# Kernel tuning notes

Hardware: AMD Instinct MI355X
Metric: run time of the kernel (lower is better)

The kernel has to match this reference:

```python
import jax, jax.numpy as jnp
import numpy as np

B, N_ROIS, C, H, W = 4, 180, 512, 48, 48
STRIDE = 4
EPS = 1e-5


def _pool_one(feat, roi):
    # feat: [C,H,W], roi: [4] float (y1,x1,y2,x2) in image coords
    r = roi / STRIDE
    r0 = jnp.trunc(r[0]).astype(jnp.int32)
    r1 = jnp.trunc(r[1]).astype(jnp.int32)
    r2 = jnp.ceil(r[2]).astype(jnp.int32)
    r3 = jnp.ceil(r[3]).astype(jnp.int32)
    h_size = r2 - r0 + 1
    w_size = r3 - r1 + 1
    idx2 = jnp.arange(2)
    # AdaptiveMaxPool2d region boundaries: [floor(i*s/2), ceil((i+1)*s/2))
    sh = (idx2 * h_size) // 2
    eh = ((idx2 + 1) * h_size + 1) // 2
    sw = (idx2 * w_size) // 2
    ew = ((idx2 + 1) * w_size + 1) // 2
    hh = jnp.arange(H)[None, :]
    ww = jnp.arange(W)[None, :]
    mask_h = (hh >= (r0 + sh)[:, None]) & (hh < (r0 + eh)[:, None])  # [2,H]
    mask_w = (ww >= (r1 + sw)[:, None]) & (ww < (r1 + ew)[:, None])  # [2,W]
    neg = jnp.finfo(feat.dtype).min
    # max over W within each col region -> [2(oj), C, H]
    mw = jnp.where(mask_w[:, None, None, :], feat[None], neg).max(axis=-1)
    # max over H within each row region -> [2(oi), 2(oj), C]
    p = jnp.where(mask_h[:, None, None, :], mw[None], neg).max(axis=-1)
    # torch layout: [C, oi, oj] then flatten row-major
    return jnp.transpose(p, (2, 0, 1)).reshape(-1)  # [C*4]


def _roi_pool(features, rois):
    # features: [B,C,H,W], rois: [B,N,4] -> [B,N,C*4]
    def per_roi(roi_b):  # roi_b: [B,4]
        return jax.vmap(_pool_one)(features, roi_b)  # [B, C*4]
    out = jax.lax.map(per_roi, jnp.swapaxes(rois, 0, 1))  # [N,B,C*4]
    return jnp.swapaxes(out, 0, 1)


def _bn(x, gamma, beta):
    # training-mode BatchNorm1d over [B, N_ROIS(channels), F]: stats over (B,F)
    mean = x.mean(axis=(0, 2), keepdims=True)
    var = ((x - mean) ** 2).mean(axis=(0, 2), keepdims=True)
    return (x - mean) * jax.lax.rsqrt(var + EPS) * gamma[None, :, None] + beta[None, :, None]


def setup_inputs() -> dict:
    key = jax.random.key(0)
    k1, k2, k3, k4, k5 = jax.random.split(key, 5)
    features = jax.random.normal(k1, (B, C, H, W), dtype=jnp.float32)
    max_coord = (H - 1) * STRIDE
    y = jnp.sort(jax.random.uniform(k2, (B, N_ROIS, 2), minval=0.0, maxval=max_coord), axis=-1)
    x = jnp.sort(jax.random.uniform(k3, (B, N_ROIS, 2), minval=0.0, maxval=max_coord), axis=-1)
    rois = jnp.stack([y[..., 0], x[..., 0], y[..., 1], x[..., 1]], axis=-1)  # [B,N,4]
    F_in = C * 4
    W1 = jax.random.normal(k4, (64, F_in), dtype=jnp.float32) * 0.02
    bl1 = jnp.zeros((64,), dtype=jnp.float32)
    gamma1 = jnp.ones((N_ROIS,), dtype=jnp.float32)
    beta1 = jnp.zeros((N_ROIS,), dtype=jnp.float32)
    gamma2 = jnp.ones((N_ROIS,), dtype=jnp.float32)
    beta2 = jnp.zeros((N_ROIS,), dtype=jnp.float32)
    return {"features": features, "rois": rois, "gamma1": gamma1, "beta1": beta1,
            "W1": W1, "bl1": bl1, "gamma2": gamma2, "beta2": beta2}


def reference(features, rois, gamma1, beta1, W1, bl1, gamma2, beta2):
    pooled = _roi_pool(features, rois)            # [B, 180, 2048]
    x = jax.nn.relu(pooled)
    x = _bn(x, gamma1, beta1)
    y = jnp.einsum('bnf,of->bno', x, W1) + bl1    # [B, 180, 64]
    y = _bn(y, gamma2, beta2)
    return y
```

## Files before the change

### kernel.cpp

```cpp
#include <hip/hip_runtime.h>
#include <hip/hip_bf16.h>
#include <cfloat>
#include <math.h>

#define BB 4
#define NR 180
#define CC 512
#define HH 48
#define WW 48
#define FF (CC*4)
#define OO 64
#define EPSV 1e-5f


typedef unsigned short us2 __attribute__((ext_vector_type(2)));

__device__ __forceinline__ unsigned pmax(unsigned a, unsigned b) {
    return __builtin_bit_cast(unsigned, __builtin_elementwise_max(
        __builtin_bit_cast(us2, a), __builtin_bit_cast(us2, b)));
}
__device__ __forceinline__ uint4 pmax4(uint4 a, uint4 b) {
    return make_uint4(pmax(a.x,b.x), pmax(a.y,b.y), pmax(a.z,b.z), pmax(a.w,b.w));
}
__device__ __forceinline__ unsigned mapb(float f) {
    unsigned fu = __float_as_uint(f);
    unsigned u = fu >> 16;
    return (fu >> 31) ? (~u & 0xFFFFu) : (u | 0x8000u);
}
__device__ __forceinline__ void unmap2(unsigned m, float& lo, float& hi) {
    unsigned t = ((~m) >> 15) & 0x00010001u;
    unsigned u = m ^ (0x80008000u ^ (t * 0x7FFFu));
    lo = __uint_as_float(u << 16);
    hi = __uint_as_float(u & 0xffff0000u);
}

__global__ __launch_bounds__(256) void k_prep(const float* __restrict__ feat,
                                              const float* __restrict__ W1,
                                              ushort* __restrict__ featB,
                                              float* __restrict__ W1T4) {
    __shared__ float tile[32][33];
    int t = threadIdx.x;
    int L = blockIdx.x;

    if (L < 4608) {
        const int S = HH * WW;
        int b   = L & 3;
        int m   = L >> 2;
        int s0  = (m % 72) * 32;
        int c0  = (m / 72) * 32;
        const float* src = feat + (size_t)b * CC * S;
        ushort* dst = featB + (size_t)b * S * CC;

        int cl = t >> 3;
        int sx = (t & 7) << 2;
        float4 v = *(const float4*)(src + (size_t)(c0 + cl) * S + s0 + sx);
        tile[cl][sx] = v.x; tile[cl][sx+1] = v.y; tile[cl][sx+2] = v.z; tile[cl][sx+3] = v.w;
        __syncthreads();

        int sl = t >> 3;
        int c4 = (t & 7) << 2;
        unsigned u0 = mapb(tile[c4][sl])   | (mapb(tile[c4+1][sl]) << 16);
        unsigned u1 = mapb(tile[c4+2][sl]) | (mapb(tile[c4+3][sl]) << 16);
        *(uint2*)(dst + (size_t)(s0 + sl) * CC + c0 + c4) = make_uint2(u0, u1);
    } else {
        int kt = L - 4608;
        int k0 = (kt >> 1) * 32, o0 = (kt & 1) * 32;
        int tx = t & 31, ty = t >> 5;
        #pragma unroll
        for (int k = 0; k < 4; k++) {
            int row = ty + k * 8;
            tile[row][tx] = W1[(size_t)(o0 + row) * FF + (k0 + tx)];
        }
        __syncthreads();
        #pragma unroll
        for (int k = 0; k < 4; k++) {
            int row = ty + k * 8;
            int kk = k0 + row;
            int o  = o0 + tx;
            W1T4[(size_t)(kk >> 2) * 256 + o * 4 + (kk & 3)] = tile[tx][row];
        }
    }
}

__global__ __launch_bounds__(512) void k_colmax(const ushort* __restrict__ featB,
                                                const float* __restrict__ rois,
                                                ushort* __restrict__ colmax) {
    __shared__ uint4 row[48 * 64];
    __shared__ int4 meta[NR];
    int b = blockIdx.x & 3;
    int h = blockIdx.x >> 2;
    int t = threadIdx.x;

    if (t < NR) {
        float4 r = ((const float4*)(rois))[b * NR + t];
        int r0 = (int)(r.x * 0.25f);
        int r1 = (int)(r.y * 0.25f);
        int r2 = (int)ceilf(r.z * 0.25f);
        int r3 = (int)ceilf(r.w * 0.25f);
        int wsz = r3 - r1 + 1;
        int ew0 = (wsz + 1) >> 1, sw1 = wsz >> 1;
        meta[t] = make_int4(r0, r2, r1, ew0 | (sw1 << 8) | (wsz << 16));
    }
    {
        const uint4* src = (const uint4*)(featB + ((size_t)(b * HH + h) * WW) * CC);
        #pragma unroll
        for (int i = 0; i < 6; i++) row[t + 512 * i] = src[t + 512 * i];
    }
    __syncthreads();

    int wv = t >> 6, lane = t & 63;
    for (int n = wv; n < NR; n += 8) {
        int4 m = meta[n];
        if (h < m.x || h > m.y) continue;
        int r1  = m.z;
        int ew0 = m.w & 255;
        int sw1 = (m.w >> 8) & 255;
        int wsz = m.w >> 16;

        uint4 s0 = make_uint4(0,0,0,0);
        {
            int w = r1, e = r1 + ew0;
            for (; w + 2 <= e; w += 2)
                s0 = pmax4(s0, pmax4(row[w * 64 + lane], row[(w + 1) * 64 + lane]));
            if (w < e) s0 = pmax4(s0, row[w * 64 + lane]);
        }
        uint4 s1 = make_uint4(0,0,0,0);
        {
            int w = r1 + sw1, e = r1 + wsz;
            for (; w + 2 <= e; w += 2)
                s1 = pmax4(s1, pmax4(row[w * 64 + lane], row[(w + 1) * 64 + lane]));
            if (w < e) s1 = pmax4(s1, row[w * 64 + lane]);
        }
        uint4* dst = (uint4*)((unsigned*)(colmax) + ((size_t)(b * NR + n) * 48 + h) * 512);
        dst[lane]      = s0;
        dst[64 + lane] = s1;
    }
}

__global__ __launch_bounds__(256) void k_rowmax(const ushort* __restrict__ colmax,
                                                const float* __restrict__ rois,
                                                ushort* __restrict__ pp) {
    __shared__ unsigned lu[4][16][64];
    int b = blockIdx.x & 3;
    int n = blockIdx.x >> 2;
    int tid = threadIdx.x;
    int g = tid >> 6, c = tid & 63;

    const float* roi = rois + ((size_t)b * NR + n) * 4;
    int r0 = (int)(roi[0] * 0.25f);
    int r2 = (int)ceilf(roi[2] * 0.25f);
    int hs  = r2 - r0 + 1;
    int eh0 = (hs + 1) >> 1, sh1 = hs >> 1;

    uint4 q00 = make_uint4(0,0,0,0), q01 = q00, q10 = q00, q11 = q00;
    const unsigned* base = (const unsigned*)(colmax) + ((size_t)(b * NR + n) * 48 + r0) * 512;
    for (int hr = g; hr < hs; hr += 4) {
        const uint4* rw = (const uint4*)(base + (size_t)hr * 512);
        uint4 s0 = rw[c];
        uint4 s1 = rw[64 + c];
        if (hr <  eh0) { q00 = pmax4(q00, s0); q01 = pmax4(q01, s1); }
        if (hr >= sh1) { q10 = pmax4(q10, s0); q11 = pmax4(q11, s1); }
    }

    {
        unsigned a, b2;
        a = q00.x; b2 = q01.x;
        lu[g][0*4 + 0][c] = (a & 0xFFFFu) | (b2 << 16);
        lu[g][0*4 + 2][c] = (a >> 16)     | (b2 & 0xFFFF0000u);
        a = q10.x; b2 = q11.x;
        lu[g][0*4 + 1][c] = (a & 0xFFFFu) | (b2 << 16);
        lu[g][0*4 + 3][c] = (a >> 16)     | (b2 & 0xFFFF0000u);
        a = q00.y; b2 = q01.y;
        lu[g][1*4 + 0][c] = (a & 0xFFFFu) | (b2 << 16);
        lu[g][1*4 + 2][c] = (a >> 16)     | (b2 & 0xFFFF0000u);
        a = q10.y; b2 = q11.y;
        lu[g][1*4 + 1][c] = (a & 0xFFFFu) | (b2 << 16);
        lu[g][1*4 + 3][c] = (a >> 16)     | (b2 & 0xFFFF0000u);
        a = q00.z; b2 = q01.z;
        lu[g][2*4 + 0][c] = (a & 0xFFFFu) | (b2 << 16);
        lu[g][2*4 + 2][c] = (a >> 16)     | (b2 & 0xFFFF0000u);
        a = q10.z; b2 = q11.z;
        lu[g][2*4 + 1][c] = (a & 0xFFFFu) | (b2 << 16);
        lu[g][2*4 + 3][c] = (a >> 16)     | (b2 & 0xFFFF0000u);
        a = q00.w; b2 = q01.w;
        lu[g][3*4 + 0][c] = (a & 0xFFFFu) | (b2 << 16);
        lu[g][3*4 + 2][c] = (a >> 16)     | (b2 & 0xFFFF0000u);
        a = q10.w; b2 = q11.w;
        lu[g][3*4 + 1][c] = (a & 0xFFFFu) | (b2 << 16);
        lu[g][3*4 + 3][c] = (a >> 16)     | (b2 & 0xFFFF0000u);
    }
    __syncthreads();

    int c2 = tid & 63, j0 = (tid >> 6) * 4;
    unsigned ou[4];
    #pragma unroll
    for (int jj = 0; jj < 4; jj++) {
        int j = j0 + jj;
        unsigned m = pmax(pmax(lu[0][j][c2], lu[1][j][c2]),
                          pmax(lu[2][j][c2], lu[3][j][c2]));
        ou[jj] = pmax(m, 0x80008000u);
    }
    unsigned* dst = (unsigned*)(pp + (size_t)(b * NR + n) * FF);
    *(uint4*)(dst + c2 * 16 + j0) = make_uint4(ou[0], ou[1], ou[2], ou[3]);
}

__global__ __launch_bounds__(1024) void k_gemm(const ushort* __restrict__ pp,
                                               const float* __restrict__ W1T4,
                                               const float* __restrict__ bl1,
                                               const float* __restrict__ g1,
                                               const float* __restrict__ b1,
                                               const float* __restrict__ g2,
                                               const float* __restrict__ b2,
                                               float* __restrict__ out) {
    __shared__ float xs[BB][FF];
    __shared__ float pd[16][BB][OO];
    __shared__ float pw[16][OO];
    __shared__ float part_s[16], part_q[16];
    __shared__ float sm2[4], sq2[4];
    int n = blockIdx.x;
    int tid = threadIdx.x;

    float s_acc = 0.f, q_acc = 0.f;
    #pragma unroll
    for (int k2 = 0; k2 < 2; k2++) {
        int gi = tid + (k2 << 10);
        int bb = gi >> 9;
        int idx = gi & 511;
        const uint2* base = (const uint2*)(pp + (size_t)(bb * NR + n) * FF);
        uint2 m = base[idx];
        float v0, v1, v2, v3;
        unmap2(m.x, v0, v1);
        unmap2(m.y, v2, v3);
        *(float4*)&xs[bb][idx << 2] = make_float4(v0, v1, v2, v3);
        s_acc += v0 + v1 + v2 + v3;
        q_acc += v0*v0 + v1*v1 + v2*v2 + v3*v3;
    }
    for (int off = 32; off; off >>= 1) {
        s_acc += __shfl_down(s_acc, off);
        q_acc += __shfl_down(q_acc, off);
    }
    if ((tid & 63) == 0) { part_s[tid >> 6] = s_acc; part_q[tid >> 6] = q_acc; }
    __syncthreads();
    float ts = 0.f, tq = 0.f;
    #pragma unroll
    for (int i = 0; i < 16; i++) { ts += part_s[i]; tq += part_q[i]; }
    const float inv1 = 1.f / (float)(BB * FF);
    float mean = ts * inv1;
    float var  = tq * inv1 - mean * mean;
    float a1n  = g1[n] * rsqrtf(var + EPSV);
    float c1n  = b1[n] - mean * a1n;

    int sc = tid >> 6;
    int o  = tid & 63;
    int k4a = sc << 5;
    float a0 = 0.f, a1 = 0.f, a2 = 0.f, a3 = 0.f, wsum = 0.f;
    #pragma unroll 4
    for (int k4 = k4a; k4 < k4a + 32; k4++) {
        float4 w4 = *(const float4*)(W1T4 + (size_t)k4 * 256 + o * 4);
        float4 x0 = *(const float4*)&xs[0][k4 << 2];
        float4 x1 = *(const float4*)&xs[1][k4 << 2];
        float4 x2 = *(const float4*)&xs[2][k4 << 2];
        float4 x3 = *(const float4*)&xs[3][k4 << 2];
        wsum += w4.x + w4.y + w4.z + w4.w;
        a0 += w4.x*x0.x + w4.y*x0.y + w4.z*x0.z + w4.w*x0.w;
        a1 += w4.x*x1.x + w4.y*x1.y + w4.z*x1.z + w4.w*x1.w;
        a2 += w4.x*x2.x + w4.y*x2.y + w4.z*x2.z + w4.w*x2.w;
        a3 += w4.x*x3.x + w4.y*x3.y + w4.z*x3.z + w4.w*x3.w;
    }
    pd[sc][0][o] = a0; pd[sc][1][o] = a1; pd[sc][2][o] = a2; pd[sc][3][o] = a3;
    pw[sc][o] = wsum;
    __syncthreads();

    float y = 0.f;
    int b = tid >> 6;
    if (tid < 256) {
        float dot = 0.f, wsm = 0.f;
        #pragma unroll
        for (int ss = 0; ss < 16; ss++) { dot += pd[ss][b][o]; wsm += pw[ss][o]; }
        y = a1n * dot + c1n * wsm + bl1[o];
        float rs = y, rq = y * y;
        for (int off = 32; off; off >>= 1) {
            rs += __shfl_down(rs, off);
            rq += __shfl_down(rq, off);
        }
        if (o == 0) { sm2[b] = rs; sq2[b] = rq; }
    }
    __syncthreads();
    if (tid < 256) {
        float sm  = sm2[0] + sm2[1] + sm2[2] + sm2[3];
        float sqm = sq2[0] + sq2[1] + sq2[2] + sq2[3];
        const float inv2 = 1.f / 256.f;
        float mean2 = sm * inv2;
        float var2  = sqm * inv2 - mean2 * mean2;
        float r2s = rsqrtf(var2 + EPSV);
        out[((size_t)b * NR + n) * OO + o] = (y - mean2) * r2s * g2[n] + b2[n];
    }
}

extern "C" void kernel_launch(void* const* d_in, const int* in_sizes, int n_in,
                              void* d_out, int out_size, void* d_ws, size_t ws_size,
                              hipStream_t stream) {
    const float* feat = (const float*)d_in[0];
    const float* rois = (const float*)d_in[1];
    const float* g1   = (const float*)d_in[2];
    const float* b1   = (const float*)d_in[3];
    const float* W1   = (const float*)d_in[4];
    const float* bl1  = (const float*)d_in[5];
    const float* g2   = (const float*)d_in[6];
    const float* b2   = (const float*)d_in[7];
    float* out = (float*)d_out;

    ushort* featB  = (ushort*)d_ws;
    float*  W1T4   = (float*)((char*)d_ws + 9437184);
    ushort* pp     = (ushort*)((char*)d_ws + 9961472);
    ushort* colmax = (ushort*)((char*)d_ws + 12910592);

    k_prep<<<4736, 256, 0, stream>>>(feat, W1, featB, W1T4);
    k_colmax<<<192, 512, 0, stream>>>(featB, rois, colmax);
    k_rowmax<<<720, 256, 0, stream>>>(colmax, rois, pp);
    k_gemm<<<NR, 1024, 0, stream>>>(pp, W1T4, bl1, g1, b1, g2, b2, out);
}
```

Baseline: 119.9 us.

## Fuse feature transpose into colmax and rowmax into gemm, cutting to two kernels

Drops the separate prep pass that converted features into a channel-last bf16-ordered buffer. The colmax kernel now reads fp32 feature rows straight from global memory and maps and transposes them into shared memory, and also handles the W1 transpose in extra blocks. The row-max reduction is folded into the gemm kernel, so the pooled intermediate no longer goes through global memory. This removes two launches and two global round trips. The cost is strided scalar shared-memory stores during the colmax load, and a gemm prologue that loops over batches with extra syncs, with only 180 blocks doing the row-max work.

```diff
diff --git a/kernel.cpp b/kernel.cpp
--- a/kernel.cpp
+++ b/kernel.cpp
@@ -22,10 +22,10 @@
 __device__ __forceinline__ uint4 pmax4(uint4 a, uint4 b) {
     return make_uint4(pmax(a.x,b.x), pmax(a.y,b.y), pmax(a.z,b.z), pmax(a.w,b.w));
 }
-__device__ __forceinline__ unsigned mapb(float f) {
+__device__ __forceinline__ ushort mapb(float f) {
     unsigned fu = __float_as_uint(f);
     unsigned u = fu >> 16;
-    return (fu >> 31) ? (~u & 0xFFFFu) : (u | 0x8000u);
+    return (ushort)((fu >> 31) ? (~u & 0xFFFFu) : (u | 0x8000u));
 }
 __device__ __forceinline__ void unmap2(unsigned m, float& lo, float& hi) {
     unsigned t = ((~m) >> 15) & 0x00010001u;
@@ -34,62 +34,45 @@
     hi = __uint_as_float(u & 0xffff0000u);
 }
 
-__global__ __launch_bounds__(256) void k_prep(const float* __restrict__ feat,
-                                              const float* __restrict__ W1,
-                                              ushort* __restrict__ featB,
-                                              float* __restrict__ W1T4) {
+__global__ __launch_bounds__(512) void k_colmax(const float* __restrict__ feat,
+                                                const float* __restrict__ rois,
+                                                const float* __restrict__ W1,
+                                                ushort* __restrict__ colmax,
+                                                float* __restrict__ W1T4) {
+    __shared__ ushort lrow[48 * 512];
+    __shared__ int4 meta[NR];
     __shared__ float tile[32][33];
+    const int S = HH * WW;
+    int blk = blockIdx.x;
     int t = threadIdx.x;
-    int L = blockIdx.x;
-
-    if (L < 4608) {
-        const int S = HH * WW;
-        int b   = L & 3;
-        int m   = L >> 2;
-        int s0  = (m % 72) * 32;
-        int c0  = (m / 72) * 32;
-        const float* src = feat + (size_t)b * CC * S;
-        ushort* dst = featB + (size_t)b * S * CC;
-
-        int cl = t >> 3;
-        int sx = (t & 7) << 2;
-        float4 v = *(const float4*)(src + (size_t)(c0 + cl) * S + s0 + sx);
-        tile[cl][sx] = v.x; tile[cl][sx+1] = v.y; tile[cl][sx+2] = v.z; tile[cl][sx+3] = v.w;
+
+    if (blk >= 192) {
+        int kt = blk - 192;
+        int k0 = (kt >> 1) * 32, o0 = (kt & 1) * 32;
+        int tx = t & 31, ty = (t >> 5) & 7;
+        bool act = (t < 256);
+        if (act) {
+            #pragma unroll
+            for (int k = 0; k < 4; k++) {
+                int row = ty + k * 8;
+                tile[row][tx] = W1[(size_t)(o0 + row) * FF + (k0 + tx)];
+            }
+        }
         __syncthreads();
-
-        int sl = t >> 3;
-        int c4 = (t & 7) << 2;
-        unsigned u0 = mapb(tile[c4][sl])   | (mapb(tile[c4+1][sl]) << 16);
-        unsigned u1 = mapb(tile[c4+2][sl]) | (mapb(tile[c4+3][sl]) << 16);
-        *(uint2*)(dst + (size_t)(s0 + sl) * CC + c0 + c4) = make_uint2(u0, u1);
-    } else {
-        int kt = L - 4608;
-        int k0 = (kt >> 1) * 32, o0 = (kt & 1) * 32;
-        int tx = t & 31, ty = t >> 5;
-        #pragma unroll
-        for (int k = 0; k < 4; k++) {
-            int row = ty + k * 8;
-            tile[row][tx] = W1[(size_t)(o0 + row) * FF + (k0 + tx)];
-        }
-        __syncthreads();
-        #pragma unroll
-        for (int k = 0; k < 4; k++) {
-            int row = ty + k * 8;
-            int kk = k0 + row;
-            int o  = o0 + tx;
-            W1T4[(size_t)(kk >> 2) * 256 + o * 4 + (kk & 3)] = tile[tx][row];
-        }
-    }
-}
-
-__global__ __launch_bounds__(512) void k_colmax(const ushort* __restrict__ featB,
-                                                const float* __restrict__ rois,
-                                                ushort* __restrict__ colmax) {
-    __shared__ uint4 row[48 * 64];
-    __shared__ int4 meta[NR];
-    int b = blockIdx.x & 3;
-    int h = blockIdx.x >> 2;
-    int t = threadIdx.x;
+        if (act) {
+            #pragma unroll
+            for (int k = 0; k < 4; k++) {
+                int row = ty + k * 8;
+                int kk = k0 + row;
+                int o  = o0 + tx;
+                W1T4[(size_t)(kk >> 2) * 256 + o * 4 + (kk & 3)] = tile[tx][row];
+            }
+        }
+        return;
+    }
+
+    int b = blk & 3;
+    int h = blk >> 2;
 
     if (t < NR) {
         float4 r = ((const float4*)(rois))[b * NR + t];
@@ -102,12 +85,22 @@
         meta[t] = make_int4(r0, r2, r1, ew0 | (sw1 << 8) | (wsz << 16));
     }
     {
-        const uint4* src = (const uint4*)(featB + ((size_t)(b * HH + h) * WW) * CC);
+        const float* src = feat + (size_t)b * CC * S + h * WW;
         #pragma unroll
-        for (int i = 0; i < 6; i++) row[t + 512 * i] = src[t + 512 * i];
-    }
-    __syncthreads();
-
+        for (int i = 0; i < 12; i++) {
+            int lin = i * 512 + t;
+            int c = lin / 12, w4 = lin - c * 12;
+            float4 v = *(const float4*)(src + (size_t)c * S + (w4 << 2));
+            int w = w4 << 2;
+            lrow[(w    ) * 512 + c] = mapb(v.x);
+            lrow[(w + 1) * 512 + c] = mapb(v.y);
+            lrow[(w + 2) * 512 + c] = mapb(v.z);
+            lrow[(w + 3) * 512 + c] = mapb(v.w);
+        }
+    }
+    __syncthreads();
+
+    const uint4* row = (const uint4*)lrow;
     int wv = t >> 6, lane = t & 63;
     for (int n = wv; n < NR; n += 8) {
         int4 m = meta[n];
@@ -137,74 +130,8 @@
     }
 }
 
-__global__ __launch_bounds__(256) void k_rowmax(const ushort* __restrict__ colmax,
-                                                const float* __restrict__ rois,
-                                                ushort* __restrict__ pp) {
-    __shared__ unsigned lu[4][16][64];
-    int b = blockIdx.x & 3;
-    int n = blockIdx.x >> 2;
-    int tid = threadIdx.x;
-    int g = tid >> 6, c = tid & 63;
-
-    const float* roi = rois + ((size_t)b * NR + n) * 4;
-    int r0 = (int)(roi[0] * 0.25f);
-    int r2 = (int)ceilf(roi[2] * 0.25f);
-    int hs  = r2 - r0 + 1;
-    int eh0 = (hs + 1) >> 1, sh1 = hs >> 1;
-
-    uint4 q00 = make_uint4(0,0,0,0), q01 = q00, q10 = q00, q11 = q00;
-    const unsigned* base = (const unsigned*)(colmax) + ((size_t)(b * NR + n) * 48 + r0) * 512;
-    for (int hr = g; hr < hs; hr += 4) {
-        const uint4* rw = (const uint4*)(base + (size_t)hr * 512);
-        uint4 s0 = rw[c];
-        uint4 s1 = rw[64 + c];
-        if (hr <  eh0) { q00 = pmax4(q00, s0); q01 = pmax4(q01, s1); }
-        if (hr >= sh1) { q10 = pmax4(q10, s0); q11 = pmax4(q11, s1); }
-    }
-
-    {
-        unsigned a, b2;
-        a = q00.x; b2 = q01.x;
-        lu[g][0*4 + 0][c] = (a & 0xFFFFu) | (b2 << 16);
-        lu[g][0*4 + 2][c] = (a >> 16)     | (b2 & 0xFFFF0000u);
-        a = q10.x; b2 = q11.x;
-        lu[g][0*4 + 1][c] = (a & 0xFFFFu) | (b2 << 16);
-        lu[g][0*4 + 3][c] = (a >> 16)     | (b2 & 0xFFFF0000u);
-        a = q00.y; b2 = q01.y;
-        lu[g][1*4 + 0][c] = (a & 0xFFFFu) | (b2 << 16);
-        lu[g][1*4 + 2][c] = (a >> 16)     | (b2 & 0xFFFF0000u);
-        a = q10.y; b2 = q11.y;
-        lu[g][1*4 + 1][c] = (a & 0xFFFFu) | (b2 << 16);
-        lu[g][1*4 + 3][c] = (a >> 16)     | (b2 & 0xFFFF0000u);
-        a = q00.z; b2 = q01.z;
-        lu[g][2*4 + 0][c] = (a & 0xFFFFu) | (b2 << 16);
-        lu[g][2*4 + 2][c] = (a >> 16)     | (b2 & 0xFFFF0000u);
-        a = q10.z; b2 = q11.z;
-        lu[g][2*4 + 1][c] = (a & 0xFFFFu) | (b2 << 16);
-        lu[g][2*4 + 3][c] = (a >> 16)     | (b2 & 0xFFFF0000u);
-        a = q00.w; b2 = q01.w;
-        lu[g][3*4 + 0][c] = (a & 0xFFFFu) | (b2 << 16);
-        lu[g][3*4 + 2][c] = (a >> 16)     | (b2 & 0xFFFF0000u);
-        a = q10.w; b2 = q11.w;
-        lu[g][3*4 + 1][c] = (a & 0xFFFFu) | (b2 << 16);
-        lu[g][3*4 + 3][c] = (a >> 16)     | (b2 & 0xFFFF0000u);
-    }
-    __syncthreads();
-
-    int c2 = tid & 63, j0 = (tid >> 6) * 4;
-    unsigned ou[4];
-    #pragma unroll
-    for (int jj = 0; jj < 4; jj++) {
-        int j = j0 + jj;
-        unsigned m = pmax(pmax(lu[0][j][c2], lu[1][j][c2]),
-                          pmax(lu[2][j][c2], lu[3][j][c2]));
-        ou[jj] = pmax(m, 0x80008000u);
-    }
-    unsigned* dst = (unsigned*)(pp + (size_t)(b * NR + n) * FF);
-    *(uint4*)(dst + c2 * 16 + j0) = make_uint4(ou[0], ou[1], ou[2], ou[3]);
-}
-
-__global__ __launch_bounds__(1024) void k_gemm(const ushort* __restrict__ pp,
+__global__ __launch_bounds__(1024) void k_gemm(const ushort* __restrict__ colmax,
+                                               const float* __restrict__ rois,
                                                const float* __restrict__ W1T4,
                                                const float* __restrict__ bl1,
                                                const float* __restrict__ g1,
@@ -213,28 +140,55 @@
                                                const float* __restrict__ b2,
                                                float* __restrict__ out) {
     __shared__ float xs[BB][FF];
+    __shared__ uint4 lds4[4][256];
     __shared__ float pd[16][BB][OO];
     __shared__ float pw[16][OO];
     __shared__ float part_s[16], part_q[16];
     __shared__ float sm2[4], sq2[4];
     int n = blockIdx.x;
     int tid = threadIdx.x;
+    int hgrp = tid >> 8;
+    int cu   = tid & 255;
 
     float s_acc = 0.f, q_acc = 0.f;
-    #pragma unroll
-    for (int k2 = 0; k2 < 2; k2++) {
-        int gi = tid + (k2 << 10);
-        int bb = gi >> 9;
-        int idx = gi & 511;
-        const uint2* base = (const uint2*)(pp + (size_t)(bb * NR + n) * FF);
-        uint2 m = base[idx];
-        float v0, v1, v2, v3;
-        unmap2(m.x, v0, v1);
-        unmap2(m.y, v2, v3);
-        *(float4*)&xs[bb][idx << 2] = make_float4(v0, v1, v2, v3);
-        s_acc += v0 + v1 + v2 + v3;
-        q_acc += v0*v0 + v1*v1 + v2*v2 + v3*v3;
-    }
+    for (int bb = 0; bb < BB; bb++) {
+        const float* roi = rois + ((size_t)bb * NR + n) * 4;
+        int r0 = (int)(roi[0] * 0.25f);
+        int r2 = (int)ceilf(roi[2] * 0.25f);
+        int hs  = r2 - r0 + 1;
+        int eh0 = (hs + 1) >> 1, sh1 = hs >> 1;
+
+        unsigned q00 = 0, q01 = 0, q10 = 0, q11 = 0;
+        const unsigned* base = (const unsigned*)(colmax) + ((size_t)(bb * NR + n) * 48 + r0) * 512;
+        for (int hr = hgrp; hr < hs; hr += 4) {
+            const unsigned* rowp = base + (size_t)hr * 512;
+            unsigned s0 = rowp[cu];
+            unsigned s1 = rowp[256 + cu];
+            if (hr <  eh0) { q00 = pmax(q00, s0); q01 = pmax(q01, s1); }
+            if (hr >= sh1) { q10 = pmax(q10, s0); q11 = pmax(q11, s1); }
+        }
+        __syncthreads();
+        lds4[hgrp][cu] = make_uint4(q00, q01, q10, q11);
+        __syncthreads();
+        if (tid < 256) {
+            uint4 m = pmax4(pmax4(lds4[0][tid], lds4[1][tid]),
+                            pmax4(lds4[2][tid], lds4[3][tid]));
+            m.x = pmax(m.x, 0x80008000u); m.y = pmax(m.y, 0x80008000u);
+            m.z = pmax(m.z, 0x80008000u); m.w = pmax(m.w, 0x80008000u);
+            float l00,h00,l01,h01,l10,h10,l11,h11;
+            unmap2(m.x, l00, h00);
+            unmap2(m.y, l01, h01);
+            unmap2(m.z, l10, h10);
+            unmap2(m.w, l11, h11);
+            int f0 = tid << 3;
+            *(float4*)&xs[bb][f0]     = make_float4(l00, l01, l10, l11);
+            *(float4*)&xs[bb][f0 + 4] = make_float4(h00, h01, h10, h11);
+            s_acc += l00 + l01 + l10 + l11 + h00 + h01 + h10 + h11;
+            q_acc += l00*l00 + l01*l01 + l10*l10 + l11*l11
+                   + h00*h00 + h01*h01 + h10*h10 + h11*h11;
+        }
+    }
+
     for (int off = 32; off; off >>= 1) {
         s_acc += __shfl_down(s_acc, off);
         q_acc += __shfl_down(q_acc, off);
@@ -310,13 +264,9 @@
     const float* b2   = (const float*)d_in[7];
     float* out = (float*)d_out;
 
-    ushort* featB  = (ushort*)d_ws;
-    float*  W1T4   = (float*)((char*)d_ws + 9437184);
-    ushort* pp     = (ushort*)((char*)d_ws + 9961472);
-    ushort* colmax = (ushort*)((char*)d_ws + 12910592);
-
-    k_prep<<<4736, 256, 0, stream>>>(feat, W1, featB, W1T4);
-    k_colmax<<<192, 512, 0, stream>>>(featB, rois, colmax);
-    k_rowmax<<<720, 256, 0, stream>>>(colmax, rois, pp);
-    k_gemm<<<NR, 1024, 0, stream>>>(pp, W1T4, bl1, g1, b1, g2, b2, out);
-}
+    float*  W1T4   = (float*)d_ws;
+    ushort* colmax = (ushort*)((char*)d_ws + 524288);
+
+    k_colmax<<<320, 512, 0, stream>>>(feat, rois, W1, colmax, W1T4);
+    k_gemm<<<NR, 1024, 0, stream>>>(colmax, rois, W1T4, bl1, g1, b1, g2, b2, out);
+}
```

After: 119.6 us. About the same (-0.2%).
